# Kernel optimization log

Measured on AMD Instinct MI355X. Metric: run time of the kernel, lower is better.

The kernel has to match this reference:

```python
import jax, jax.numpy as jnp
import numpy as np

B, S, E, H = 8, 2048, 384, 6
D = E // H  # head dim = 64


def setup_inputs() -> dict:
    key = jax.random.key(0)
    ks = jax.random.split(key, 5)
    s = 1.0 / np.sqrt(E)
    return {
        "x": jax.random.normal(ks[0], (B, S, E), dtype=jnp.float32),
        "Wq": jax.random.normal(ks[1], (E, E), dtype=jnp.float32) * s,
        "Wk": jax.random.normal(ks[2], (E, E), dtype=jnp.float32) * s,
        "Wv": jax.random.normal(ks[3], (E, E), dtype=jnp.float32) * s,
        "Wo": jax.random.normal(ks[4], (E, E), dtype=jnp.float32) * s,
        "bo": jnp.zeros((E,), dtype=jnp.float32),
    }


def reference(x, Wq, Wk, Wv, Wo, bo):
    b, s, e = x.shape
    # QKV projections (torch Linear with bias=False: x @ W.T; here W stored as [in,out])
    q = (x @ Wq).reshape(b, s, H, D).transpose(0, 2, 1, 3)  # [b,h,s,d]
    k = (x @ Wk).reshape(b, s, H, D).transpose(0, 2, 1, 3)
    v = (x @ Wv).reshape(b, s, H, D).transpose(0, 2, 1, 3)
    scores = jnp.einsum("bhqd,bhkd->bhqk", q, k) / jnp.sqrt(jnp.asarray(D, x.dtype))
    causal = jnp.tril(jnp.ones((s, s), dtype=bool))
    scores = jnp.where(causal, scores, -jnp.inf)
    attn = jax.nn.softmax(scores, axis=-1)
    # NOTE: original applies dropout but then uses the PRE-dropout softmax for @V,
    # so dropout is a no-op; we faithfully omit it.
    out = jnp.einsum("bhqk,bhkd->bhqd", attn, v)  # [b,h,s,d]
    out = out.transpose(0, 2, 1, 3).reshape(b, s, e)
    return out @ Wo + bo
```

## Files before the change

kernel.cpp:

```cpp
#include <hip/hip_runtime.h>
#include <hip/hip_bf16.h>
#include <cstdint>
#include <cstddef>

typedef __attribute__((ext_vector_type(8))) short short8;
typedef __attribute__((ext_vector_type(4))) float f32x4;

#define S_LEN 2048
#define EMB 384
#define NH 6
#define HD 64
#define NB 8
#define QSCALE 0.180336880f

__device__ __forceinline__ unsigned short f2bf(float f) {
  return __builtin_bit_cast(unsigned short, __float2bfloat16(f));
}

__global__ __launch_bounds__(256) void k_prepw(
    const float* __restrict__ Wq, const float* __restrict__ Wk,
    const float* __restrict__ Wv, const float* __restrict__ Wo,
    unsigned short* __restrict__ Wqt, unsigned short* __restrict__ Wkt,
    unsigned short* __restrict__ Wvt, unsigned short* __restrict__ Wot) {
  __shared__ unsigned short Lw[64 * 66];
  const int tid = threadIdx.x;
  const int bx2 = blockIdx.x;
  const int mat = bx2 / 36;
  const int tile = bx2 - mat * 36;
  const int k0 = (tile / 6) * 64;
  const int n0 = (tile % 6) * 64;
  const float* W = (mat == 0) ? Wq : (mat == 1) ? Wk : (mat == 2) ? Wv : Wo;
  unsigned short* Wt = (mat == 0) ? Wqt : (mat == 1) ? Wkt : (mat == 2) ? Wvt : Wot;
  const int f4 = tid & 15;
#pragma unroll
  for (int it = 0; it < 4; ++it) {
    const int kl = it * 16 + (tid >> 4);
    const float4 v = reinterpret_cast<const float4*>(W + (size_t)(k0 + kl) * EMB + n0)[f4];
    Lw[kl * 66 + f4 * 4 + 0] = f2bf(v.x);
    Lw[kl * 66 + f4 * 4 + 1] = f2bf(v.y);
    Lw[kl * 66 + f4 * 4 + 2] = f2bf(v.z);
    Lw[kl * 66 + f4 * 4 + 3] = f2bf(v.w);
  }
  __syncthreads();
  const int g = tid & 7;
#pragma unroll
  for (int it = 0; it < 2; ++it) {
    const int nl = it * 32 + (tid >> 3);
    short8 o;
#pragma unroll
    for (int j = 0; j < 8; ++j) o[j] = (short)Lw[(g * 8 + j) * 66 + nl];
    *reinterpret_cast<short8*>(Wt + (size_t)(n0 + nl) * EMB + k0 + g * 8) = o;
  }
}

__global__ __launch_bounds__(256) void k_qkv(
    const float* __restrict__ x,
    const unsigned short* __restrict__ Wqt,
    const unsigned short* __restrict__ Wkt,
    const unsigned short* __restrict__ Wvt,
    unsigned short* __restrict__ Qb,
    unsigned short* __restrict__ Kb,
    unsigned short* __restrict__ Vtb) {
  __shared__ __attribute__((aligned(16))) unsigned short La[128 * 72];
  __shared__ __attribute__((aligned(16))) unsigned short Lt[64 * 136];

  const int tid = threadIdx.x;
  const int lane = tid & 63;
  const int w = tid >> 6;
  const int wr = w >> 1, wc = w & 1;
  const int lr = lane & 15, lg = lane >> 4;

  const int bid = blockIdx.y * 128 + blockIdx.x;
  const int xcd = bid & 7;
  const int pos = bid >> 3;
  const int bx = xcd * 16 + (pos & 15);
  const int by = pos >> 4;
  const int m0 = bx * 128;
  const int wsel = by / 3;
  const int n0 = (by % 3) * 128;
  const unsigned short* Wt = (wsel == 0) ? Wqt : (wsel == 1) ? Wkt : Wvt;

  const int srow = tid >> 3;
  const int sg = tid & 7;

  f32x4 acc[4][4] = {};
  float4 xf[4][2];
  short8 breg[2][2][4];

#pragma unroll
  for (int i = 0; i < 4; ++i) {
    const float* src = x + (size_t)(m0 + i * 32 + srow) * EMB + sg * 8;
    xf[i][0] = *reinterpret_cast<const float4*>(src);
    xf[i][1] = *reinterpret_cast<const float4*>(src + 4);
  }
#pragma unroll
  for (int kk = 0; kk < 2; ++kk)
#pragma unroll
    for (int ns = 0; ns < 4; ++ns)
      breg[0][kk][ns] = *reinterpret_cast<const short8*>(
          Wt + (size_t)(n0 + wc * 64 + ns * 16 + lr) * EMB + kk * 32 + lg * 8);

#pragma unroll
  for (int kt = 0; kt < 6; ++kt) {
    const int cur = kt & 1, nxt = cur ^ 1;
    __syncthreads();
#pragma unroll
    for (int i = 0; i < 4; ++i) {
      short8 v;
      v[0] = (short)f2bf(xf[i][0].x); v[1] = (short)f2bf(xf[i][0].y);
      v[2] = (short)f2bf(xf[i][0].z); v[3] = (short)f2bf(xf[i][0].w);
      v[4] = (short)f2bf(xf[i][1].x); v[5] = (short)f2bf(xf[i][1].y);
      v[6] = (short)f2bf(xf[i][1].z); v[7] = (short)f2bf(xf[i][1].w);
      *reinterpret_cast<short8*>(&La[(i * 32 + srow) * 72 + sg * 8]) = v;
    }
    __syncthreads();
    if (kt < 5) {
      const int kn = (kt + 1) * 64;
#pragma unroll
      for (int i = 0; i < 4; ++i) {
        const float* src = x + (size_t)(m0 + i * 32 + srow) * EMB + kn + sg * 8;
        xf[i][0] = *reinterpret_cast<const float4*>(src);
        xf[i][1] = *reinterpret_cast<const float4*>(src + 4);
      }
#pragma unroll
      for (int kk = 0; kk < 2; ++kk)
#pragma unroll
        for (int ns = 0; ns < 4; ++ns)
          breg[nxt][kk][ns] = *reinterpret_cast<const short8*>(
              Wt + (size_t)(n0 + wc * 64 + ns * 16 + lr) * EMB + kn + kk * 32 + lg * 8);
    }
#pragma unroll
    for (int kk = 0; kk < 2; ++kk) {
      short8 a[4];
#pragma unroll
      for (int ms = 0; ms < 4; ++ms)
        a[ms] = *reinterpret_cast<const short8*>(
            &La[(wr * 64 + ms * 16 + lr) * 72 + kk * 32 + lg * 8]);
#pragma unroll
      for (int ms = 0; ms < 4; ++ms)
#pragma unroll
        for (int ns = 0; ns < 4; ++ns)
          acc[ms][ns] = __builtin_amdgcn_mfma_f32_16x16x32_bf16(
              a[ms], breg[cur][kk][ns], acc[ms][ns], 0, 0, 0);
    }
  }

  const int bb = m0 >> 11;
  const int s0 = m0 & 2047;
  if (wsel != 2) {
    unsigned short* Out = (wsel == 0) ? Qb : Kb;
    const float sc = (wsel == 0) ? QSCALE : 1.0f;
#pragma unroll
    for (int p = 0; p < 2; ++p) {
      __syncthreads();
      if (wr == p) {
#pragma unroll
        for (int ms = 0; ms < 4; ++ms)
#pragma unroll
          for (int ns = 0; ns < 4; ++ns)
#pragma unroll
            for (int r = 0; r < 4; ++r)
              Lt[(ms * 16 + lg * 4 + r) * 136 + wc * 64 + ns * 16 + lr] =
                  f2bf(acc[ms][ns][r] * sc);
      }
      __syncthreads();
#pragma unroll
      for (int it = 0; it < 4; ++it) {
        const int row = (tid >> 3) + 32 * (it & 1);
        const int ch = (tid & 7) + 8 * (it >> 1);
        const short8 v = *reinterpret_cast<const short8*>(&Lt[row * 136 + ch * 8]);
        const int n = n0 + ch * 8;
        const int h = n >> 6, d = n & 63;
        *reinterpret_cast<short8*>(
            Out + (((size_t)bb * NH + h) * S_LEN + (s0 + p * 64 + row)) * HD + d) = v;
      }
    }
  } else {
#pragma unroll
    for (int p = 0; p < 2; ++p) {
      __syncthreads();
      if (wc == p) {
#pragma unroll
        for (int ms = 0; ms < 4; ++ms)
#pragma unroll
          for (int ns = 0; ns < 4; ++ns)
#pragma unroll
            for (int r = 0; r < 4; ++r) {
              const int dl = ns * 16 + lr;
              const int ml = wr * 64 + ms * 16 + lg * 4 + r;
              Lt[dl * 136 + (((ml >> 3) ^ (dl & 7)) << 3) + (ml & 7)] = f2bf(acc[ms][ns][r]);
            }
      }
      __syncthreads();
      const int hg = 2 * (n0 >> 7) + p;
      const int c = tid & 15;
#pragma unroll
      for (int it = 0; it < 4; ++it) {
        const int d = it * 16 + (tid >> 4);
        const short8 v = *reinterpret_cast<const short8*>(
            &Lt[d * 136 + ((c ^ (d & 7)) << 3)]);
        *reinterpret_cast<short8*>(
            Vtb + (((size_t)bb * NH + hg) * HD + d) * S_LEN + s0 + c * 8) = v;
      }
    }
  }
}

__device__ __forceinline__ void attn_step(
    const unsigned short* __restrict__ K, const unsigned short* __restrict__ V,
    unsigned short* __restrict__ Ps,
    const short8 aq0, const short8 aq1,
    const int t, const int qt, const int qbase,
    const int w, const int lr, const int lg,
    f32x4* o, float* l_i) {
  const bool diag = (t == qt);
  const int kkmax = diag ? ((w >> 1) + 1) : 2;
  const int ksmax = kkmax * 2;

  float sv[4][4];
#pragma unroll
  for (int ks = 0; ks < 4; ++ks) {
    if (!diag || ks <= w) {
      const int krow = ks * 16 + lr;
      const int kx = krow & 7;
      const short8 bk0 = *reinterpret_cast<const short8*>(&K[krow * 64 + ((lg ^ kx) << 3)]);
      const short8 bk1 = *reinterpret_cast<const short8*>(&K[krow * 64 + (((4 + lg) ^ kx) << 3)]);
      f32x4 s = {};
      s = __builtin_amdgcn_mfma_f32_16x16x32_bf16(aq0, bk0, s, 0, 0, 0);
      s = __builtin_amdgcn_mfma_f32_16x16x32_bf16(aq1, bk1, s, 0, 0, 0);
      if (diag && ks == w) {
#pragma unroll
        for (int r = 0; r < 4; ++r)
          sv[ks][r] = (lr <= lg * 4 + r) ? s[r] : -1e30f;
      } else {
#pragma unroll
        for (int r = 0; r < 4; ++r) sv[ks][r] = s[r];
      }
    }
  }

#pragma unroll
  for (int r = 0; r < 4; ++r) {
    const int q = w * 16 + lg * 4 + r;
    const int qx = q & 7;
    const int abase = q * 64 + (lr & 7);
    const int sp = lr >> 3;
    float s = 0.f;
#pragma unroll
    for (int ks = 0; ks < 4; ++ks) {
      if (!diag || ks <= w) {
        const float p = __builtin_amdgcn_exp2f(sv[ks][r]);
        s += p;
        Ps[abase + ((((ks << 1) | sp) ^ qx) << 3)] = f2bf(p);
      } else if (ks < ksmax) {
        Ps[abase + ((((ks << 1) | sp) ^ qx) << 3)] = 0;
      }
    }
    l_i[r] += s;
  }

  const int qrow = w * 16 + lr;
  const int qx2 = qrow & 7;
#pragma unroll
  for (int kk = 0; kk < 2; ++kk) {
    if (kk < kkmax) {
      const short8 ap = *reinterpret_cast<const short8*>(
          &Ps[qrow * 64 + (((kk * 4 + lg) ^ qx2) << 3)]);
#pragma unroll
      for (int ns = 0; ns < 4; ++ns) {
        const int vrow = ns * 16 + lr;
        const short8 bv = *reinterpret_cast<const short8*>(
            &V[vrow * 64 + (((kk * 4 + lg) ^ (vrow & 7)) << 3)]);
        o[ns] = __builtin_amdgcn_mfma_f32_16x16x32_bf16(ap, bv, o[ns], 0, 0, 0);
      }
    }
  }
}

__global__ __launch_bounds__(256, 3) void k_attn(
    const unsigned short* __restrict__ Qb,
    const unsigned short* __restrict__ Kb,
    const unsigned short* __restrict__ Vtg,
    unsigned short* __restrict__ Ob) {
  __shared__ __attribute__((aligned(16))) unsigned short Ksb[2][64 * 64];
  __shared__ __attribute__((aligned(16))) unsigned short Vtb[2][64 * 64];
  __shared__ __attribute__((aligned(16))) unsigned short Psb[2][64 * 64];

  const int tid = threadIdx.x;
  const int lane = tid & 63;
  const int w = tid >> 6;
  const int lr = lane & 15, lg = lane >> 4;

  const int lin = blockIdx.y * 16 + blockIdx.x;
  const int swz = (lin & 7) * 96 + (lin >> 3);
  const int idx = swz & 15;
  const int bh = swz >> 4;
  const int pair = (idx & 1) ? (15 - (idx >> 1)) : (idx >> 1);
  const int qtA = pair, qtB = 31 - pair;

  const unsigned short* Qp = Qb + (size_t)bh * S_LEN * HD;
  const unsigned short* Kp = Kb + (size_t)bh * S_LEN * HD;
  const unsigned short* Vp = Vtg + (size_t)bh * S_LEN * HD;
  const int b = bh / NH, hh = bh - b * NH;

  const int srow = tid >> 3;
  const int sslot = tid & 7;
  const int wsl0 = (sslot ^ (srow & 7)) << 3;

  const int qbA = qtA * 64 + w * 16;
  const int qbB = qtB * 64 + w * 16;

  const short8 aqA0 = *reinterpret_cast<const short8*>(Qp + (size_t)(qbA + lr) * HD + lg * 8);
  const short8 aqA1 = *reinterpret_cast<const short8*>(Qp + (size_t)(qbA + lr) * HD + 32 + lg * 8);
  const short8 aqB0 = *reinterpret_cast<const short8*>(Qp + (size_t)(qbB + lr) * HD + lg * 8);
  const short8 aqB1 = *reinterpret_cast<const short8*>(Qp + (size_t)(qbB + lr) * HD + 32 + lg * 8);

  f32x4 oA[4] = {}, oB[4] = {};
  float lA[4] = {0.f, 0.f, 0.f, 0.f}, lB[4] = {0.f, 0.f, 0.f, 0.f};

  short8 pk0 = *reinterpret_cast<const short8*>(Kp + (size_t)srow * HD + sslot * 8);
  short8 pk1 = *reinterpret_cast<const short8*>(Kp + (size_t)(srow + 32) * HD + sslot * 8);
  short8 pv0 = *reinterpret_cast<const short8*>(Vp + (size_t)srow * S_LEN + sslot * 8);
  short8 pv1 = *reinterpret_cast<const short8*>(Vp + (size_t)(srow + 32) * S_LEN + sslot * 8);
  *reinterpret_cast<short8*>(&Ksb[0][srow * 64 + wsl0]) = pk0;
  *reinterpret_cast<short8*>(&Ksb[0][(srow + 32) * 64 + wsl0]) = pk1;
  *reinterpret_cast<short8*>(&Vtb[0][srow * 64 + wsl0]) = pv0;
  *reinterpret_cast<short8*>(&Vtb[0][(srow + 32) * 64 + wsl0]) = pv1;
  __syncthreads();

  for (int t = 0; t <= qtB; ++t) {
    const int cur = t & 1;
    const bool more = t < qtB;
    if (more) {
      const int tn = (t + 1) * 64;
      pk0 = *reinterpret_cast<const short8*>(Kp + (size_t)(tn + srow) * HD + sslot * 8);
      pk1 = *reinterpret_cast<const short8*>(Kp + (size_t)(tn + srow + 32) * HD + sslot * 8);
      pv0 = *reinterpret_cast<const short8*>(Vp + (size_t)srow * S_LEN + tn + sslot * 8);
      pv1 = *reinterpret_cast<const short8*>(Vp + (size_t)(srow + 32) * S_LEN + tn + sslot * 8);
    }

    attn_step(Ksb[cur], Vtb[cur], Psb[1], aqB0, aqB1, t, qtB, qbB, w, lr, lg, oB, lB);
    if (t <= qtA)
      attn_step(Ksb[cur], Vtb[cur], Psb[0], aqA0, aqA1, t, qtA, qbA, w, lr, lg, oA, lA);

    if (more) {
      const int nxt = cur ^ 1;
      *reinterpret_cast<short8*>(&Ksb[nxt][srow * 64 + wsl0]) = pk0;
      *reinterpret_cast<short8*>(&Ksb[nxt][(srow + 32) * 64 + wsl0]) = pk1;
      *reinterpret_cast<short8*>(&Vtb[nxt][srow * 64 + wsl0]) = pv0;
      *reinterpret_cast<short8*>(&Vtb[nxt][(srow + 32) * 64 + wsl0]) = pv1;
    }
    __syncthreads();
  }

#pragma unroll
  for (int r = 0; r < 4; ++r) {
    float la = lA[r], lb = lB[r];
    la += __shfl_xor(la, 1); lb += __shfl_xor(lb, 1);
    la += __shfl_xor(la, 2); lb += __shfl_xor(lb, 2);
    la += __shfl_xor(la, 4); lb += __shfl_xor(lb, 4);
    la += __shfl_xor(la, 8); lb += __shfl_xor(lb, 8);
    lA[r] = 1.0f / la; lB[r] = 1.0f / lb;
  }
#pragma unroll
  for (int ns = 0; ns < 4; ++ns)
#pragma unroll
    for (int r = 0; r < 4; ++r) {
      const int qgA = qbA + lg * 4 + r;
      const int qgB = qbB + lg * 4 + r;
      Ob[((size_t)(b * S_LEN + qgA)) * EMB + hh * HD + ns * 16 + lr] = f2bf(oA[ns][r] * lA[r]);
      Ob[((size_t)(b * S_LEN + qgB)) * EMB + hh * HD + ns * 16 + lr] = f2bf(oB[ns][r] * lB[r]);
    }
}

__global__ __launch_bounds__(256) void k_oproj(
    const unsigned short* __restrict__ Ob,
    const unsigned short* __restrict__ Wot,
    const float* __restrict__ bo,
    float* __restrict__ out) {
  __shared__ __attribute__((aligned(16))) unsigned short La[64 * 72];
  __shared__ __attribute__((aligned(16))) float Lf[64 * 132];

  const int tid = threadIdx.x;
  const int lane = tid & 63;
  const int w = tid >> 6;
  const int lr = lane & 15, lg = lane >> 4;

  const int bid = blockIdx.y * 256 + blockIdx.x;
  const int xcd = bid & 7;
  const int pos = bid >> 3;
  const int m0 = (xcd * 32 + (pos & 31)) * 64;
  const int n0 = (pos >> 5) * 128;

  const int srow = tid >> 3;
  const int sg = tid & 7;

  f32x4 acc[4][2] = {};
  short8 st[2];
  short8 breg[2][2][2];

#pragma unroll
  for (int i = 0; i < 2; ++i)
    st[i] = *reinterpret_cast<const short8*>(
        Ob + (size_t)(m0 + i * 32 + srow) * EMB + sg * 8);
#pragma unroll
  for (int kk = 0; kk < 2; ++kk)
#pragma unroll
    for (int ns = 0; ns < 2; ++ns)
      breg[0][kk][ns] = *reinterpret_cast<const short8*>(
          Wot + (size_t)(n0 + w * 32 + ns * 16 + lr) * EMB + kk * 32 + lg * 8);

#pragma unroll
  for (int kt = 0; kt < 6; ++kt) {
    const int cur = kt & 1, nxt = cur ^ 1;
    __syncthreads();
#pragma unroll
    for (int i = 0; i < 2; ++i)
      *reinterpret_cast<short8*>(&La[(i * 32 + srow) * 72 + sg * 8]) = st[i];
    __syncthreads();
    if (kt < 5) {
      const int kn = (kt + 1) * 64;
#pragma unroll
      for (int i = 0; i < 2; ++i)
        st[i] = *reinterpret_cast<const short8*>(
            Ob + (size_t)(m0 + i * 32 + srow) * EMB + kn + sg * 8);
#pragma unroll
      for (int kk = 0; kk < 2; ++kk)
#pragma unroll
        for (int ns = 0; ns < 2; ++ns)
          breg[nxt][kk][ns] = *reinterpret_cast<const short8*>(
              Wot + (size_t)(n0 + w * 32 + ns * 16 + lr) * EMB + kn + kk * 32 + lg * 8);
    }
#pragma unroll
    for (int kk = 0; kk < 2; ++kk) {
      short8 a[4];
#pragma unroll
      for (int ms = 0; ms < 4; ++ms)
        a[ms] = *reinterpret_cast<const short8*>(
            &La[(ms * 16 + lr) * 72 + kk * 32 + lg * 8]);
#pragma unroll
      for (int ms = 0; ms < 4; ++ms)
#pragma unroll
        for (int ns = 0; ns < 2; ++ns)
          acc[ms][ns] = __builtin_amdgcn_mfma_f32_16x16x32_bf16(
              a[ms], breg[cur][kk][ns], acc[ms][ns], 0, 0, 0);
    }
  }

  __syncthreads();
#pragma unroll
  for (int ms = 0; ms < 4; ++ms)
#pragma unroll
    for (int ns = 0; ns < 2; ++ns)
#pragma unroll
      for (int r = 0; r < 4; ++r)
        Lf[(ms * 16 + lg * 4 + r) * 132 + w * 32 + ns * 16 + lr] = acc[ms][ns][r];
  __syncthreads();
#pragma unroll
  for (int it = 0; it < 8; ++it) {
    const int row = (tid >> 3) + 32 * (it & 1);
    const int c4 = (tid & 7) + 8 * (it >> 1);
    float4 v = *reinterpret_cast<const float4*>(&Lf[row * 132 + c4 * 4]);
    const float4 b4 = *reinterpret_cast<const float4*>(&bo[n0 + c4 * 4]);
    v.x += b4.x; v.y += b4.y; v.z += b4.z; v.w += b4.w;
    *reinterpret_cast<float4*>(&out[(size_t)(m0 + row) * EMB + n0 + c4 * 4]) = v;
  }
}

extern "C" void kernel_launch(void* const* d_in, const int* in_sizes, int n_in,
                              void* d_out, int out_size, void* d_ws, size_t ws_size,
                              hipStream_t stream) {
  const float* x  = (const float*)d_in[0];
  const float* Wq = (const float*)d_in[1];
  const float* Wk = (const float*)d_in[2];
  const float* Wv = (const float*)d_in[3];
  const float* Wo = (const float*)d_in[4];
  const float* bo = (const float*)d_in[5];
  float* out = (float*)d_out;

  uint8_t* ws = (uint8_t*)d_ws;
  unsigned short* Wqt = (unsigned short*)(ws + 12582912);
  unsigned short* Wkt = (unsigned short*)(ws + 12877824);
  unsigned short* Wvt = (unsigned short*)(ws + 13172736);
  unsigned short* Wot = (unsigned short*)(ws + 13467648);
  unsigned short* Qb  = (unsigned short*)(ws + 13762560);
  unsigned short* Kb  = (unsigned short*)(ws + 26345472);
  unsigned short* VT  = (unsigned short*)(ws + 38928384);
  unsigned short* Ob  = (unsigned short*)(ws + 51511296);

  hipLaunchKernelGGL(k_prepw, dim3(144), dim3(256), 0, stream,
                     Wq, Wk, Wv, Wo, Wqt, Wkt, Wvt, Wot);
  hipLaunchKernelGGL(k_qkv, dim3(128, 9), dim3(256), 0, stream,
                     x, Wqt, Wkt, Wvt, Qb, Kb, VT);
  hipLaunchKernelGGL(k_attn, dim3(16, 48), dim3(256), 0, stream, Qb, Kb, VT, Ob);
  hipLaunchKernelGGL(k_oproj, dim3(256, 3), dim3(256), 0, stream, Ob, Wot, bo, out);
}
```

Baseline: 191.1 us.

## Compute transposed QK^T, share K/V fragments across both query tiles

The attention inner loop now loads K and V fragments from shared memory once per tile and reuses them for both query tiles A and B, rather than reloading them per call. QK^T is computed transposed (K as the A operand), so each lane holds four consecutive key probabilities for one query row. Those are packed and written to the P buffer as one 8-byte store instead of four scalar stores. The row sum becomes a single scalar per lane, reduced across lane groups at the end. This cuts LDS traffic and store instructions, but keeping the fragment arrays live raises register pressure under the 3-blocks launch bound.

```diff
diff --git a/kernel.cpp b/kernel.cpp
--- a/kernel.cpp
+++ b/kernel.cpp
@@ -206,77 +206,6 @@
   }
 }
 
-__device__ __forceinline__ void attn_step(
-    const unsigned short* __restrict__ K, const unsigned short* __restrict__ V,
-    unsigned short* __restrict__ Ps,
-    const short8 aq0, const short8 aq1,
-    const int t, const int qt, const int qbase,
-    const int w, const int lr, const int lg,
-    f32x4* o, float* l_i) {
-  const bool diag = (t == qt);
-  const int kkmax = diag ? ((w >> 1) + 1) : 2;
-  const int ksmax = kkmax * 2;
-
-  float sv[4][4];
-#pragma unroll
-  for (int ks = 0; ks < 4; ++ks) {
-    if (!diag || ks <= w) {
-      const int krow = ks * 16 + lr;
-      const int kx = krow & 7;
-      const short8 bk0 = *reinterpret_cast<const short8*>(&K[krow * 64 + ((lg ^ kx) << 3)]);
-      const short8 bk1 = *reinterpret_cast<const short8*>(&K[krow * 64 + (((4 + lg) ^ kx) << 3)]);
-      f32x4 s = {};
-      s = __builtin_amdgcn_mfma_f32_16x16x32_bf16(aq0, bk0, s, 0, 0, 0);
-      s = __builtin_amdgcn_mfma_f32_16x16x32_bf16(aq1, bk1, s, 0, 0, 0);
-      if (diag && ks == w) {
-#pragma unroll
-        for (int r = 0; r < 4; ++r)
-          sv[ks][r] = (lr <= lg * 4 + r) ? s[r] : -1e30f;
-      } else {
-#pragma unroll
-        for (int r = 0; r < 4; ++r) sv[ks][r] = s[r];
-      }
-    }
-  }
-
-#pragma unroll
-  for (int r = 0; r < 4; ++r) {
-    const int q = w * 16 + lg * 4 + r;
-    const int qx = q & 7;
-    const int abase = q * 64 + (lr & 7);
-    const int sp = lr >> 3;
-    float s = 0.f;
-#pragma unroll
-    for (int ks = 0; ks < 4; ++ks) {
-      if (!diag || ks <= w) {
-        const float p = __builtin_amdgcn_exp2f(sv[ks][r]);
-        s += p;
-        Ps[abase + ((((ks << 1) | sp) ^ qx) << 3)] = f2bf(p);
-      } else if (ks < ksmax) {
-        Ps[abase + ((((ks << 1) | sp) ^ qx) << 3)] = 0;
-      }
-    }
-    l_i[r] += s;
-  }
-
-  const int qrow = w * 16 + lr;
-  const int qx2 = qrow & 7;
-#pragma unroll
-  for (int kk = 0; kk < 2; ++kk) {
-    if (kk < kkmax) {
-      const short8 ap = *reinterpret_cast<const short8*>(
-          &Ps[qrow * 64 + (((kk * 4 + lg) ^ qx2) << 3)]);
-#pragma unroll
-      for (int ns = 0; ns < 4; ++ns) {
-        const int vrow = ns * 16 + lr;
-        const short8 bv = *reinterpret_cast<const short8*>(
-            &V[vrow * 64 + (((kk * 4 + lg) ^ (vrow & 7)) << 3)]);
-        o[ns] = __builtin_amdgcn_mfma_f32_16x16x32_bf16(ap, bv, o[ns], 0, 0, 0);
-      }
-    }
-  }
-}
-
 __global__ __launch_bounds__(256, 3) void k_attn(
     const unsigned short* __restrict__ Qb,
     const unsigned short* __restrict__ Kb,
@@ -284,7 +213,8 @@
     unsigned short* __restrict__ Ob) {
   __shared__ __attribute__((aligned(16))) unsigned short Ksb[2][64 * 64];
   __shared__ __attribute__((aligned(16))) unsigned short Vtb[2][64 * 64];
-  __shared__ __attribute__((aligned(16))) unsigned short Psb[2][64 * 64];
+  __shared__ __attribute__((aligned(16))) unsigned short PsA[64 * 64];
+  __shared__ __attribute__((aligned(16))) unsigned short PsB[64 * 64];
 
   const int tid = threadIdx.x;
   const int lane = tid & 63;
@@ -316,7 +246,12 @@
   const short8 aqB1 = *reinterpret_cast<const short8*>(Qp + (size_t)(qbB + lr) * HD + 32 + lg * 8);
 
   f32x4 oA[4] = {}, oB[4] = {};
-  float lA[4] = {0.f, 0.f, 0.f, 0.f}, lB[4] = {0.f, 0.f, 0.f, 0.f};
+  float lA = 0.f, lB = 0.f;
+
+  const int prow = (w * 16 + lr) * 64;
+  const int pmask = lr & 7;
+  const int ph = (lg & 1) * 4;
+  const int ptb = lg >> 1;
 
   short8 pk0 = *reinterpret_cast<const short8*>(Kp + (size_t)srow * HD + sslot * 8);
   short8 pk1 = *reinterpret_cast<const short8*>(Kp + (size_t)(srow + 32) * HD + sslot * 8);
@@ -339,9 +274,83 @@
       pv1 = *reinterpret_cast<const short8*>(Vp + (size_t)(srow + 32) * S_LEN + tn + sslot * 8);
     }
 
-    attn_step(Ksb[cur], Vtb[cur], Psb[1], aqB0, aqB1, t, qtB, qbB, w, lr, lg, oB, lB);
-    if (t <= qtA)
-      attn_step(Ksb[cur], Vtb[cur], Psb[0], aqA0, aqA1, t, qtA, qbA, w, lr, lg, oA, lA);
+    const unsigned short* Ks = Ksb[cur];
+    const unsigned short* Vt = Vtb[cur];
+    const bool doA = (t <= qtA);
+    const bool diagA = (t == qtA);
+    const bool diagB = (t == qtB);
+
+    short8 kf0[4], kf1[4];
+#pragma unroll
+    for (int ks = 0; ks < 4; ++ks) {
+      const int krow = ks * 16 + lr;
+      const int kx = krow & 7;
+      kf0[ks] = *reinterpret_cast<const short8*>(&Ks[krow * 64 + ((lg ^ kx) << 3)]);
+      kf1[ks] = *reinterpret_cast<const short8*>(&Ks[krow * 64 + (((4 + lg) ^ kx) << 3)]);
+    }
+
+    auto qkt_set = [&](const short8& aq0, const short8& aq1,
+                       unsigned short* Ps, float& lsum, const bool diag) {
+      const int kkm2 = diag ? (((w >> 1) + 1) << 1) : 4;
+#pragma unroll
+      for (int ks = 0; ks < 4; ++ks) {
+        unsigned short* pp = Ps + prow + (((2 * ks + ptb) ^ pmask) << 3) + ph;
+        if (!diag || ks <= w) {
+          f32x4 s = {};
+          s = __builtin_amdgcn_mfma_f32_16x16x32_bf16(kf0[ks], aq0, s, 0, 0, 0);
+          s = __builtin_amdgcn_mfma_f32_16x16x32_bf16(kf1[ks], aq1, s, 0, 0, 0);
+          float p[4];
+          if (diag && ks == w) {
+#pragma unroll
+            for (int r = 0; r < 4; ++r)
+              p[r] = (4 * lg + r <= lr) ? __builtin_amdgcn_exp2f(s[r]) : 0.f;
+          } else {
+#pragma unroll
+            for (int r = 0; r < 4; ++r) p[r] = __builtin_amdgcn_exp2f(s[r]);
+          }
+          lsum += (p[0] + p[1]) + (p[2] + p[3]);
+          uint2 pkd;
+          pkd.x = ((unsigned)f2bf(p[1]) << 16) | (unsigned)f2bf(p[0]);
+          pkd.y = ((unsigned)f2bf(p[3]) << 16) | (unsigned)f2bf(p[2]);
+          *reinterpret_cast<uint2*>(pp) = pkd;
+        } else if (ks < kkm2) {
+          *reinterpret_cast<uint2*>(pp) = make_uint2(0u, 0u);
+        }
+      }
+    };
+
+    qkt_set(aqB0, aqB1, PsB, lB, diagB);
+    if (doA) qkt_set(aqA0, aqA1, PsA, lA, diagA);
+
+    short8 vf0[4], vf1[4];
+#pragma unroll
+    for (int ns = 0; ns < 4; ++ns) {
+      const int vrow = ns * 16 + lr;
+      const int vx = vrow & 7;
+      vf0[ns] = *reinterpret_cast<const short8*>(&Vt[vrow * 64 + ((lg ^ vx) << 3)]);
+      vf1[ns] = *reinterpret_cast<const short8*>(&Vt[vrow * 64 + (((4 + lg) ^ vx) << 3)]);
+    }
+
+    auto pv_set = [&](const unsigned short* Ps, f32x4* o, const bool diag) {
+      const int kkm = diag ? ((w >> 1) + 1) : 2;
+      {
+        const short8 ap = *reinterpret_cast<const short8*>(
+            &Ps[prow + ((lg ^ pmask) << 3)]);
+#pragma unroll
+        for (int ns = 0; ns < 4; ++ns)
+          o[ns] = __builtin_amdgcn_mfma_f32_16x16x32_bf16(ap, vf0[ns], o[ns], 0, 0, 0);
+      }
+      if (kkm > 1) {
+        const short8 ap = *reinterpret_cast<const short8*>(
+            &Ps[prow + (((4 + lg) ^ pmask) << 3)]);
+#pragma unroll
+        for (int ns = 0; ns < 4; ++ns)
+          o[ns] = __builtin_amdgcn_mfma_f32_16x16x32_bf16(ap, vf1[ns], o[ns], 0, 0, 0);
+      }
+    };
+
+    pv_set(PsB, oB, diagB);
+    if (doA) pv_set(PsA, oA, diagA);
 
     if (more) {
       const int nxt = cur ^ 1;
@@ -353,14 +362,15 @@
     __syncthreads();
   }
 
+  lA += __shfl_xor(lA, 16); lA += __shfl_xor(lA, 32);
+  lB += __shfl_xor(lB, 16); lB += __shfl_xor(lB, 32);
+  const float liA = 1.0f / lA;
+  const float liB = 1.0f / lB;
+  float liAr[4], liBr[4];
 #pragma unroll
   for (int r = 0; r < 4; ++r) {
-    float la = lA[r], lb = lB[r];
-    la += __shfl_xor(la, 1); lb += __shfl_xor(lb, 1);
-    la += __shfl_xor(la, 2); lb += __shfl_xor(lb, 2);
-    la += __shfl_xor(la, 4); lb += __shfl_xor(lb, 4);
-    la += __shfl_xor(la, 8); lb += __shfl_xor(lb, 8);
-    lA[r] = 1.0f / la; lB[r] = 1.0f / lb;
+    liAr[r] = __shfl(liA, 4 * lg + r);
+    liBr[r] = __shfl(liB, 4 * lg + r);
   }
 #pragma unroll
   for (int ns = 0; ns < 4; ++ns)
@@ -368,8 +378,8 @@
     for (int r = 0; r < 4; ++r) {
       const int qgA = qbA + lg * 4 + r;
       const int qgB = qbB + lg * 4 + r;
-      Ob[((size_t)(b * S_LEN + qgA)) * EMB + hh * HD + ns * 16 + lr] = f2bf(oA[ns][r] * lA[r]);
-      Ob[((size_t)(b * S_LEN + qgB)) * EMB + hh * HD + ns * 16 + lr] = f2bf(oB[ns][r] * lB[r]);
+      Ob[((size_t)(b * S_LEN + qgA)) * EMB + hh * HD + ns * 16 + lr] = f2bf(oA[ns][r] * liAr[r]);
+      Ob[((size_t)(b * S_LEN + qgB)) * EMB + hh * HD + ns * 16 + lr] = f2bf(oB[ns][r] * liBr[r]);
     }
 }
 
```

New measurement: 183.9 us. 3.8% less time.
